# Kernel optimization log

Measured on AMD Instinct MI355X. Metric: run time of the kernel, lower is better.

Reference implementation:

```python
import jax, jax.numpy as jnp
import numpy as np

BN_EPS = 1e-5


def setup_inputs() -> dict:
    key = jax.random.key(0)
    k1, k2, k3 = jax.random.split(key, 3)
    n, d = 4096, 128
    x = jax.random.normal(k1, (2 * n, d), dtype=jnp.float32)
    affinity_A = jax.random.normal(k2, (n, n), dtype=jnp.float32)
    # Xavier-uniform-like init for the [d, d] weight
    lim = float(np.sqrt(6.0 / (d + d)))
    weight = jax.random.uniform(k3, (d, d), dtype=jnp.float32, minval=-lim, maxval=lim)
    gamma = jnp.ones((d,), dtype=jnp.float32)
    beta = jnp.zeros((d,), dtype=jnp.float32)
    return {"x": x, "affinity_A": affinity_A, "weight": weight, "gamma": gamma, "beta": beta}


def reference(x, affinity_A, weight, gamma, beta):
    # Binarize affinity
    A = jnp.where(affinity_A > 0, 1.0, 0.0).astype(x.dtype)  # [n, n]
    n = A.shape[0]
    I = jnp.eye(n, dtype=x.dtype)
    # Block adjacency [[A, I], [I, A]] -> [2n, 2n]
    adj = jnp.block([[A, I], [I, A]])
    # Symmetric normalization D^{-1/2} A D^{-1/2}.
    # (Original code materializes D^{-1/2} as a full matrix and does two O(n^3)
    # matmuls; mathematically it is just row/column scaling, done here directly.)
    deg = adj.sum(axis=1)                 # [2n], >= 1 because of identity blocks
    dinv = deg ** -0.5
    norm_A = dinv[:, None] * adj * dinv[None, :]
    # GCN propagation: (norm_A @ x) @ W
    h = (norm_A @ x) @ weight             # [2n, d]
    # BatchNorm1d (training mode, biased variance) + ReLU
    mean = h.mean(axis=0)
    var = h.var(axis=0)
    h = (h - mean) * jax.lax.rsqrt(var + BN_EPS) * gamma + beta
    return jax.nn.relu(h)
```

## Files before the change

kernel.cpp:

```cpp
#include <hip/hip_runtime.h>
#include <stdint.h>


#define N_NODES 4096
#define D 128
#define TWO_N (2*N_NODES)

typedef unsigned short u16;
typedef unsigned int u32;
typedef __bf16 bf16;
typedef bf16 bf16x8 __attribute__((ext_vector_type(8)));
typedef float f32x4 __attribute__((ext_vector_type(4)));
typedef u16 u16x8 __attribute__((ext_vector_type(8)));

__device__ __forceinline__ float bf2f(u16 u) {
    return __builtin_bit_cast(float, ((unsigned)u) << 16);
}
__device__ __forceinline__ u16 f2bf(float f) {
    unsigned b = __builtin_bit_cast(unsigned, f);
    unsigned r = (b + 0x7FFFu + ((b >> 16) & 1u)) >> 16;
    return (u16)r;
}
__device__ __forceinline__ bool det_fp32(const u16* gamma) {
    return gamma[0] != (u16)0x3F80;
}

__global__ void k_degscale(const void* __restrict__ x, const void* __restrict__ aff,
                           const void* __restrict__ W, const u16* __restrict__ gamma,
                           float* __restrict__ dinv, u16* __restrict__ XsT,
                           u16* __restrict__ WT, unsigned char* __restrict__ Abits) {
    int t = threadIdx.x;
    bool fp32 = det_fp32(gamma);
    const u16* W16 = (const u16*)W;
    const float* W32 = (const float*)W;

    if (blockIdx.x >= 256) {
        int o = (blockIdx.x - 256) * 16 + (t >> 4);
        int cg = (t & 15) * 8;
        u16x8 wv;
        #pragma unroll
        for (int e = 0; e < 8; ++e) {
            size_t wi = (size_t)(cg + e) * D + o;
            float v = fp32 ? W32[wi] : bf2f(W16[wi]);
            wv[e] = f2bf(v);
        }
        *reinterpret_cast<u16x8*>(WT + (size_t)o * D + cg) = wv;
        return;
    }

    __shared__ int scnt[16];
    __shared__ float sdinv[16];
    int wid = t >> 6, lane = t & 63;
    int j0 = blockIdx.x * 16;

    int cnt[4] = {0, 0, 0, 0};
    if (!fp32) {
        const u16* base = (const u16*)aff + (size_t)(j0 + wid * 4) * N_NODES;
        #pragma unroll
        for (int r = 0; r < 4; ++r) {
            unsigned char* ab = Abits + (size_t)(j0 + wid * 4 + r) * 512 + lane;
            #pragma unroll
            for (int it = 0; it < 8; ++it) {
                u16x8 v = *reinterpret_cast<const u16x8*>(base + (size_t)r * N_NODES + it * 512 + lane * 8);
                unsigned bb = 0;
                #pragma unroll
                for (int e = 0; e < 8; ++e) bb |= ((short)v[e] > 0) ? (1u << e) : 0u;
                cnt[r] += __builtin_popcount(bb);
                ab[it * 64] = (unsigned char)bb;
            }
        }
    } else {
        const float* base = (const float*)aff + (size_t)(j0 + wid * 4) * N_NODES;
        #pragma unroll
        for (int r = 0; r < 4; ++r) {
            unsigned char* ab = Abits + (size_t)(j0 + wid * 4 + r) * 512 + lane;
            #pragma unroll
            for (int it = 0; it < 8; ++it) {
                f32x4 va = *reinterpret_cast<const f32x4*>(base + (size_t)r * N_NODES + it * 512 + lane * 8);
                f32x4 vb = *reinterpret_cast<const f32x4*>(base + (size_t)r * N_NODES + it * 512 + lane * 8 + 4);
                unsigned bb = 0;
                #pragma unroll
                for (int e = 0; e < 4; ++e) {
                    bb |= (va[e] > 0.f) ? (1u << e) : 0u;
                    bb |= (vb[e] > 0.f) ? (1u << (4 + e)) : 0u;
                }
                cnt[r] += __builtin_popcount(bb);
                ab[it * 64] = (unsigned char)bb;
            }
        }
    }
    #pragma unroll
    for (int r = 0; r < 4; ++r) {
        int c = cnt[r];
        #pragma unroll
        for (int off = 32; off; off >>= 1) c += __shfl_down(c, off, 64);
        if (lane == 0) scnt[wid * 4 + r] = c;
    }
    __syncthreads();
    if (t < 16) {
        float d = rsqrtf((float)(scnt[t] + 1));
        sdinv[t] = d;
        dinv[j0 + t] = d;
    }
    __syncthreads();

    int cc = t & 127;
    const u16* xb16 = (const u16*)x + ((t < 128) ? (size_t)0 : (size_t)N_NODES * D);
    const float* xb32 = (const float*)x + ((t < 128) ? (size_t)0 : (size_t)N_NODES * D);
    u16x8 b0, b1;
    #pragma unroll
    for (int jl = 0; jl < 8; ++jl) {
        size_t xi = (size_t)(j0 + jl) * D + cc;
        float xv = fp32 ? xb32[xi] : bf2f(xb16[xi]);
        b0[jl] = f2bf(sdinv[jl] * xv);
    }
    #pragma unroll
    for (int jl = 0; jl < 8; ++jl) {
        size_t xi = (size_t)(j0 + 8 + jl) * D + cc;
        float xv = fp32 ? xb32[xi] : bf2f(xb16[xi]);
        b1[jl] = f2bf(sdinv[8 + jl] * xv);
    }
    int kb = j0 >> 5, qd = (j0 >> 3) & 3, cg = t >> 4, r15 = t & 15;
    size_t idx0 = (((size_t)kb * 16 + cg) * 64 + qd * 16 + r15) * 8;
    *reinterpret_cast<u16x8*>(XsT + idx0) = b0;
    *reinterpret_cast<u16x8*>(XsT + idx0 + 128) = b1;
}

#define SK 4
#define KCHUNK (N_NODES / SK)
#define LDA 72

#define PREFB(KK, PBV)                                                              \
    {                                                                               \
        _Pragma("unroll")                                                           \
        for (int ks = 0; ks < 2; ++ks) {                                            \
            _Pragma("unroll")                                                       \
            for (int j = 0; j < 4; ++j)                                             \
                PBV[ks * 4 + j] = *reinterpret_cast<const u16x8*>(                  \
                    pB0 + ((KK) * 2 + ks) * 8192 + j * 512);                        \
        }                                                                           \
    }

#define MFMA_PHASE(BUF, PBV)                                                        \
    {                                                                               \
        _Pragma("unroll")                                                           \
        for (int ks = 0; ks < 2; ++ks) {                                            \
            bf16x8 af[4];                                                           \
            _Pragma("unroll")                                                       \
            for (int i = 0; i < 4; ++i)                                             \
                af[i] = *reinterpret_cast<const bf16x8*>(                           \
                    &sA[BUF][(i * 16 + l15) * LDA + ks * 32 + quad * 8]);           \
            _Pragma("unroll")                                                       \
            for (int j = 0; j < 4; ++j) {                                           \
                bf16x8 bfr = __builtin_bit_cast(bf16x8, PBV[ks * 4 + j]);           \
                _Pragma("unroll")                                                   \
                for (int i = 0; i < 4; ++i)                                         \
                    acc[i][j] = __builtin_amdgcn_mfma_f32_16x16x32_bf16(            \
                        af[i], bfr, acc[i][j], 0, 0, 0);                            \
            }                                                                       \
        }                                                                           \
    }

__launch_bounds__(256, 1)
__global__ void k_gemm(const unsigned char* __restrict__ Abits, const u16* __restrict__ XsT,
                       u16* __restrict__ Ypart) {
    __shared__ unsigned char sBits[64 * 128];
    __shared__ u16 sA[2][64 * LDA];
    int tid = threadIdx.x;
    int mt = blockIdx.x >> 2;
    int sk = blockIdx.x & 3;
    int rm0 = mt * 64;
    int lane = tid & 63, wid = tid >> 6;
    int quad = lane >> 4, l15 = lane & 15;

    f32x4 acc[4][4];
    #pragma unroll
    for (int i = 0; i < 4; ++i)
        #pragma unroll
        for (int j = 0; j < 4; ++j) acc[i][j] = (f32x4){0.f, 0.f, 0.f, 0.f};

    {
        int r = tid >> 2, seg = tid & 3;
        const unsigned char* g = Abits + (size_t)(rm0 + r) * 512 + sk * 128 + seg * 32;
        u16x8 lo = *reinterpret_cast<const u16x8*>(g);
        u16x8 hi = *reinterpret_cast<const u16x8*>(g + 16);
        int swz = (r & 7) << 4;
        *reinterpret_cast<u16x8*>(sBits + r * 128 + ((seg * 32) ^ swz)) = lo;
        *reinterpret_cast<u16x8*>(sBits + r * 128 + ((seg * 32 + 16) ^ swz)) = hi;
    }

    int er = tid & 63, eq = tid >> 6;
    int eswz = (er & 7) << 4;
    auto expand = [&](int kk, int buf) {
        u16 w = *reinterpret_cast<const u16*>(sBits + er * 128 + (((kk << 3) + eq * 2) ^ eswz));
        u32 out[8];
        #pragma unroll
        for (int m = 0; m < 8; ++m)
            out[m] = ((w >> (2 * m)) & 1u) * 0x3F80u
                   | (u32)((w >> (2 * m + 1)) & 1u) * 0x3F800000u;
        *reinterpret_cast<u16x8*>(&sA[buf][er * LDA + eq * 16]) =
            *reinterpret_cast<u16x8*>(&out[0]);
        *reinterpret_cast<u16x8*>(&sA[buf][er * LDA + eq * 16 + 8]) =
            *reinterpret_cast<u16x8*>(&out[4]);
    };

    const u16* pB0 = XsT + (((size_t)sk * 512 + wid * 4) * 64 + lane) * 8;

    u16x8 pbA[8], pbB[8];
    __syncthreads();
    expand(0, 0);
    PREFB(0, pbA);

    for (int kk = 0; kk < 16; kk += 2) {
        __syncthreads();
        PREFB(kk + 1, pbB);
        expand(kk + 1, 1);
        MFMA_PHASE(0, pbA);
        __syncthreads();
        if (kk + 2 < 16) {
            PREFB(kk + 2, pbA);
            expand(kk + 2, 0);
        }
        MFMA_PHASE(1, pbB);
    }

    u16* yp = Ypart + (size_t)sk * N_NODES * 256;
    #pragma unroll
    for (int i = 0; i < 4; ++i) {
        int row = rm0 + i * 16 + quad * 4;
        #pragma unroll
        for (int j = 0; j < 4; ++j) {
            int col = wid * 64 + j * 16 + l15;
            #pragma unroll
            for (int r = 0; r < 4; ++r)
                yp[(size_t)(row + r) * 256 + col] = f2bf(acc[i][j][r]);
        }
    }
}

__global__ void k_comb(const u16* __restrict__ Ypart, const void* __restrict__ x,
                       const u16* __restrict__ WT, const u16* __restrict__ gamma,
                       const float* __restrict__ dinv, u16* __restrict__ hpre,
                       float* __restrict__ pS, float* __restrict__ pQ) {
    __shared__ u16 sH[32 * 136];
    __shared__ u16 sWT[128 * 136];
    __shared__ float sOut[32 * 132];
    int t = threadIdx.x;
    bool fp32 = det_fp32(gamma);
    int r0 = blockIdx.x * 32;
    bool top = blockIdx.x < 128;
    int node0 = top ? r0 : r0 - N_NODES;
    const u16* x16 = (const u16*)x;
    const float* x32 = (const float*)x;

    #pragma unroll
    for (int p = 0; p < 2; ++p) {
        int r = (t >> 4) + p * 16;
        int c0 = (t & 15) * 8;
        int node = node0 + r;
        int ycol = (top ? 0 : 128) + c0;
        float fs[8] = {0.f, 0.f, 0.f, 0.f, 0.f, 0.f, 0.f, 0.f};
        #pragma unroll
        for (int sk = 0; sk < SK; ++sk) {
            u16x8 yv = *reinterpret_cast<const u16x8*>(Ypart + ((size_t)sk * N_NODES + node) * 256 + ycol);
            #pragma unroll
            for (int e = 0; e < 8; ++e) fs[e] += bf2f(yv[e]);
        }
        float dv = dinv[node];
        size_t xi = (top ? (size_t)(N_NODES + node) : (size_t)node) * D + c0;
        u16x8 hv;
        if (!fp32) {
            u16x8 xv = *reinterpret_cast<const u16x8*>(x16 + xi);
            #pragma unroll
            for (int e = 0; e < 8; ++e) hv[e] = f2bf(dv * fs[e] + dv * dv * bf2f(xv[e]));
        } else {
            f32x4 xa = *reinterpret_cast<const f32x4*>(x32 + xi);
            f32x4 xb = *reinterpret_cast<const f32x4*>(x32 + xi + 4);
            #pragma unroll
            for (int e = 0; e < 4; ++e) {
                hv[e]     = f2bf(dv * fs[e]     + dv * dv * xa[e]);
                hv[4 + e] = f2bf(dv * fs[4 + e] + dv * dv * xb[e]);
            }
        }
        *reinterpret_cast<u16x8*>(sH + r * 136 + c0) = hv;
    }
    #pragma unroll
    for (int p = 0; p < 8; ++p) {
        int idx = p * 256 + t;
        int o = idx >> 4;
        int cg = (idx & 15) * 8;
        u16x8 wv = *reinterpret_cast<const u16x8*>(WT + (size_t)o * D + cg);
        *reinterpret_cast<u16x8*>(sWT + o * 136 + cg) = wv;
    }
    __syncthreads();

    int lane = t & 63, wid = t >> 6;
    int wm = wid >> 1, wn = wid & 1;
    int quad = lane >> 4, l15 = lane & 15;
    f32x4 acc[4];
    #pragma unroll
    for (int j = 0; j < 4; ++j) acc[j] = (f32x4){0.f, 0.f, 0.f, 0.f};
    #pragma unroll
    for (int ks = 0; ks < 4; ++ks) {
        bf16x8 af = *reinterpret_cast<const bf16x8*>(sH + (wm * 16 + l15) * 136 + ks * 32 + quad * 8);
        #pragma unroll
        for (int j = 0; j < 4; ++j) {
            bf16x8 bfr = *reinterpret_cast<const bf16x8*>(sWT + (wn * 64 + j * 16 + l15) * 136 + ks * 32 + quad * 8);
            acc[j] = __builtin_amdgcn_mfma_f32_16x16x32_bf16(af, bfr, acc[j], 0, 0, 0);
        }
    }
    #pragma unroll
    for (int j = 0; j < 4; ++j) {
        int row = wm * 16 + quad * 4;
        int col = wn * 64 + j * 16 + l15;
        #pragma unroll
        for (int r = 0; r < 4; ++r) sOut[(row + r) * 132 + col] = acc[j][r];
    }
    __syncthreads();
    #pragma unroll
    for (int p = 0; p < 16; ++p) {
        int idx = p * 256 + t;
        int r = idx >> 7, c = idx & 127;
        hpre[(size_t)(r0 + r) * D + c] = f2bf(sOut[r * 132 + c]);
    }
    if (t < 128) {
        float s = 0.f, q = 0.f;
        #pragma unroll
        for (int r = 0; r < 32; ++r) {
            float v = sOut[r * 132 + t];
            s += v; q += v * v;
        }
        pS[blockIdx.x * 128 + t] = s;
        pQ[blockIdx.x * 128 + t] = q;
    }
}

__global__ void k_stats(const float* __restrict__ pS, const float* __restrict__ pQ,
                        const void* __restrict__ gamma, const void* __restrict__ beta,
                        const u16* __restrict__ gdet, float* __restrict__ scsh) {
    __shared__ float rs[256], rq[256];
    int t = threadIdx.x;
    int c0 = blockIdx.x * 8;
    int cl = t & 7;
    int rr = t >> 3;
    float s = 0.f, q = 0.f;
    #pragma unroll
    for (int i = 0; i < 8; ++i) {
        int row = rr + i * 32;
        s += pS[row * 128 + c0 + cl];
        q += pQ[row * 128 + c0 + cl];
    }
    rs[t] = s; rq[t] = q;
    __syncthreads();
    #pragma unroll
    for (int st = 128; st >= 8; st >>= 1) {
        if (t < st) { rs[t] += rs[t + st]; rq[t] += rq[t + st]; }
        __syncthreads();
    }
    if (t < 8) {
        bool fp32 = det_fp32(gdet);
        int c = c0 + t;
        float mean = rs[t] * (1.0f / TWO_N);
        float var = fmaxf(rq[t] * (1.0f / TWO_N) - mean * mean, 0.f);
        float inv = rsqrtf(var + 1e-5f);
        float g = fp32 ? ((const float*)gamma)[c] : bf2f(((const u16*)gamma)[c]);
        float b = fp32 ? ((const float*)beta)[c]  : bf2f(((const u16*)beta)[c]);
        scsh[c] = inv * g;
        scsh[128 + c] = b - mean * inv * g;
    }
}

__global__ void k_bn(const u16* __restrict__ hpre, const float* __restrict__ scsh,
                     const u16* __restrict__ gdet, void* __restrict__ out) {
    __shared__ float ssc[128], ssh[128];
    int t = threadIdx.x;
    bool fp32 = det_fp32(gdet);
    if (t < 128) { ssc[t] = scsh[t]; ssh[t] = scsh[128 + t]; }
    __syncthreads();
    size_t base = (size_t)blockIdx.x * 2048 + t * 8;
    int c0 = (t & 15) * 8;
    u16x8 hv = *reinterpret_cast<const u16x8*>(hpre + base);
    if (!fp32) {
        u16x8 ov;
        #pragma unroll
        for (int e = 0; e < 8; ++e) {
            float v = bf2f(hv[e]) * ssc[c0 + e] + ssh[c0 + e];
            ov[e] = f2bf(fmaxf(v, 0.f));
        }
        *reinterpret_cast<u16x8*>((u16*)out + base) = ov;
    } else {
        float* o = (float*)out + base;
        #pragma unroll
        for (int e = 0; e < 8; ++e) {
            float v = bf2f(hv[e]) * ssc[c0 + e] + ssh[c0 + e];
            o[e] = fmaxf(v, 0.f);
        }
    }
}

extern "C" void kernel_launch(void* const* d_in, const int* in_sizes, int n_in,
                              void* d_out, int out_size, void* d_ws, size_t ws_size,
                              hipStream_t stream) {
    const void* x = d_in[0];
    const void* aff = d_in[1];
    const void* W = d_in[2];
    const u16* gamma = (const u16*)d_in[3];
    const void* beta = d_in[4];

    char* ws = (char*)d_ws;
    u16* XsT = (u16*)ws;
    u16* hpre = XsT;
    u16* Ypart = (u16*)(ws + 2097152);
    float* dinv = (float*)(ws + 10485760);
    float* pS = (float*)(ws + 10502144);
    float* pQ = (float*)(ws + 10633216);
    float* scsh = (float*)(ws + 10764288);
    u16* WT = (u16*)(ws + 10765312);
    unsigned char* Abits = (unsigned char*)(ws + 10798080);

    k_degscale<<<264, 256, 0, stream>>>(x, aff, W, gamma, dinv, XsT, WT, Abits);
    k_gemm<<<256, 256, 0, stream>>>(Abits, XsT, Ypart);
    k_comb<<<256, 256, 0, stream>>>(Ypart, x, WT, gamma, dinv, hpre, pS, pQ);
    k_stats<<<16, 256, 0, stream>>>(pS, pQ, gamma, beta, gamma, scsh);
    k_bn<<<512, 256, 0, stream>>>(hpre, scsh, gamma, d_out);
}
```

Before: 133.1 us.

## Halve rows per degscale block and load pre-swizzled W fragments directly into registers

The degree/bit-packing kernel now handles 8 rows per block instead of 16 and launches twice as many blocks, raising parallelism across CUs for the memory-bound binarization pass. The transposed weight is written in an MFMA-fragment-ready order, so the combine kernel loads B fragments straight from global memory into registers. This drops the 34 KB shared-memory staging of W and one LDS round trip, at the cost of more registers per thread and redundant global reads of W across blocks.

```diff
diff --git a/kernel.cpp b/kernel.cpp
--- a/kernel.cpp
+++ b/kernel.cpp
@@ -34,8 +34,10 @@
     const u16* W16 = (const u16*)W;
     const float* W32 = (const float*)W;
 
-    if (blockIdx.x >= 256) {
-        int o = (blockIdx.x - 256) * 16 + (t >> 4);
+    if (blockIdx.x >= 512) {
+        int b = blockIdx.x - 512;
+        int ol = t >> 4;
+        int o = b * 16 + ol;
         int cg = (t & 15) * 8;
         u16x8 wv;
         #pragma unroll
@@ -44,21 +46,22 @@
             float v = fp32 ? W32[wi] : bf2f(W16[wi]);
             wv[e] = f2bf(v);
         }
-        *reinterpret_cast<u16x8*>(WT + (size_t)o * D + cg) = wv;
+        int ks = cg >> 5, qc = (cg >> 3) & 3;
+        *reinterpret_cast<u16x8*>(WT + (size_t)((ks * 8 + b) * 64 + qc * 16 + ol) * 8) = wv;
         return;
     }
 
-    __shared__ int scnt[16];
-    __shared__ float sdinv[16];
+    __shared__ int scnt[8];
+    __shared__ float sdinv[8];
     int wid = t >> 6, lane = t & 63;
-    int j0 = blockIdx.x * 16;
-
-    int cnt[4] = {0, 0, 0, 0};
+    int j0 = blockIdx.x * 8;
+
+    int cnt[2] = {0, 0};
     if (!fp32) {
-        const u16* base = (const u16*)aff + (size_t)(j0 + wid * 4) * N_NODES;
-        #pragma unroll
-        for (int r = 0; r < 4; ++r) {
-            unsigned char* ab = Abits + (size_t)(j0 + wid * 4 + r) * 512 + lane;
+        const u16* base = (const u16*)aff + (size_t)(j0 + wid * 2) * N_NODES;
+        #pragma unroll
+        for (int r = 0; r < 2; ++r) {
+            unsigned char* ab = Abits + (size_t)(j0 + wid * 2 + r) * 512 + lane;
             #pragma unroll
             for (int it = 0; it < 8; ++it) {
                 u16x8 v = *reinterpret_cast<const u16x8*>(base + (size_t)r * N_NODES + it * 512 + lane * 8);
@@ -70,10 +73,10 @@
             }
         }
     } else {
-        const float* base = (const float*)aff + (size_t)(j0 + wid * 4) * N_NODES;
-        #pragma unroll
-        for (int r = 0; r < 4; ++r) {
-            unsigned char* ab = Abits + (size_t)(j0 + wid * 4 + r) * 512 + lane;
+        const float* base = (const float*)aff + (size_t)(j0 + wid * 2) * N_NODES;
+        #pragma unroll
+        for (int r = 0; r < 2; ++r) {
+            unsigned char* ab = Abits + (size_t)(j0 + wid * 2 + r) * 512 + lane;
             #pragma unroll
             for (int it = 0; it < 8; ++it) {
                 f32x4 va = *reinterpret_cast<const f32x4*>(base + (size_t)r * N_NODES + it * 512 + lane * 8);
@@ -90,14 +93,14 @@
         }
     }
     #pragma unroll
-    for (int r = 0; r < 4; ++r) {
+    for (int r = 0; r < 2; ++r) {
         int c = cnt[r];
         #pragma unroll
         for (int off = 32; off; off >>= 1) c += __shfl_down(c, off, 64);
-        if (lane == 0) scnt[wid * 4 + r] = c;
-    }
-    __syncthreads();
-    if (t < 16) {
+        if (lane == 0) scnt[wid * 2 + r] = c;
+    }
+    __syncthreads();
+    if (t < 8) {
         float d = rsqrtf((float)(scnt[t] + 1));
         sdinv[t] = d;
         dinv[j0 + t] = d;
@@ -107,23 +110,15 @@
     int cc = t & 127;
     const u16* xb16 = (const u16*)x + ((t < 128) ? (size_t)0 : (size_t)N_NODES * D);
     const float* xb32 = (const float*)x + ((t < 128) ? (size_t)0 : (size_t)N_NODES * D);
-    u16x8 b0, b1;
+    u16x8 b0;
     #pragma unroll
     for (int jl = 0; jl < 8; ++jl) {
         size_t xi = (size_t)(j0 + jl) * D + cc;
         float xv = fp32 ? xb32[xi] : bf2f(xb16[xi]);
         b0[jl] = f2bf(sdinv[jl] * xv);
     }
-    #pragma unroll
-    for (int jl = 0; jl < 8; ++jl) {
-        size_t xi = (size_t)(j0 + 8 + jl) * D + cc;
-        float xv = fp32 ? xb32[xi] : bf2f(xb16[xi]);
-        b1[jl] = f2bf(sdinv[8 + jl] * xv);
-    }
     int kb = j0 >> 5, qd = (j0 >> 3) & 3, cg = t >> 4, r15 = t & 15;
-    size_t idx0 = (((size_t)kb * 16 + cg) * 64 + qd * 16 + r15) * 8;
-    *reinterpret_cast<u16x8*>(XsT + idx0) = b0;
-    *reinterpret_cast<u16x8*>(XsT + idx0 + 128) = b1;
+    *reinterpret_cast<u16x8*>(XsT + (((size_t)kb * 16 + cg) * 64 + qd * 16 + r15) * 8) = b0;
 }
 
 #define SK 4
@@ -243,7 +238,6 @@
                        const float* __restrict__ dinv, u16* __restrict__ hpre,
                        float* __restrict__ pS, float* __restrict__ pQ) {
     __shared__ u16 sH[32 * 136];
-    __shared__ u16 sWT[128 * 136];
     __shared__ float sOut[32 * 132];
     int t = threadIdx.x;
     bool fp32 = det_fp32(gamma);
@@ -253,6 +247,18 @@
     const u16* x16 = (const u16*)x;
     const float* x32 = (const float*)x;
 
+    int lane = t & 63, wid = t >> 6;
+    int wm = wid >> 1, wn = wid & 1;
+    int quad = lane >> 4, l15 = lane & 15;
+
+    u16x8 wf[4][4];
+    #pragma unroll
+    for (int ks = 0; ks < 4; ++ks)
+        #pragma unroll
+        for (int j = 0; j < 4; ++j)
+            wf[ks][j] = *reinterpret_cast<const u16x8*>(
+                WT + (size_t)((ks * 8 + wn * 4 + j) * 64 + lane) * 8);
+
     #pragma unroll
     for (int p = 0; p < 2; ++p) {
         int r = (t >> 4) + p * 16;
@@ -284,19 +290,8 @@
         }
         *reinterpret_cast<u16x8*>(sH + r * 136 + c0) = hv;
     }
-    #pragma unroll
-    for (int p = 0; p < 8; ++p) {
-        int idx = p * 256 + t;
-        int o = idx >> 4;
-        int cg = (idx & 15) * 8;
-        u16x8 wv = *reinterpret_cast<const u16x8*>(WT + (size_t)o * D + cg);
-        *reinterpret_cast<u16x8*>(sWT + o * 136 + cg) = wv;
-    }
-    __syncthreads();
-
-    int lane = t & 63, wid = t >> 6;
-    int wm = wid >> 1, wn = wid & 1;
-    int quad = lane >> 4, l15 = lane & 15;
+    __syncthreads();
+
     f32x4 acc[4];
     #pragma unroll
     for (int j = 0; j < 4; ++j) acc[j] = (f32x4){0.f, 0.f, 0.f, 0.f};
@@ -305,7 +300,7 @@
         bf16x8 af = *reinterpret_cast<const bf16x8*>(sH + (wm * 16 + l15) * 136 + ks * 32 + quad * 8);
         #pragma unroll
         for (int j = 0; j < 4; ++j) {
-            bf16x8 bfr = *reinterpret_cast<const bf16x8*>(sWT + (wn * 64 + j * 16 + l15) * 136 + ks * 32 + quad * 8);
+            bf16x8 bfr = __builtin_bit_cast(bf16x8, wf[ks][j]);
             acc[j] = __builtin_amdgcn_mfma_f32_16x16x32_bf16(af, bfr, acc[j], 0, 0, 0);
         }
     }
@@ -418,7 +413,7 @@
     u16* WT = (u16*)(ws + 10765312);
     unsigned char* Abits = (unsigned char*)(ws + 10798080);
 
-    k_degscale<<<264, 256, 0, stream>>>(x, aff, W, gamma, dinv, XsT, WT, Abits);
+    k_degscale<<<520, 256, 0, stream>>>(x, aff, W, gamma, dinv, XsT, WT, Abits);
     k_gemm<<<256, 256, 0, stream>>>(Abits, XsT, Ypart);
     k_comb<<<256, 256, 0, stream>>>(Ypart, x, WT, gamma, dinv, hpre, pS, pQ);
     k_stats<<<16, 256, 0, stream>>>(pS, pQ, gamma, beta, gamma, scsh);
```

Measured after the change: 131.3 us, median of 2. Within noise of the previous version (-1.3%).
